# Optimization experiments

Hardware: AMD Instinct MI355X
Metric: run time of the kernel (lower is better)

The kernel has to match this reference:

```python
import jax, jax.numpy as jnp
import numpy as np

# constants matching init_kwargs
WINDOW_SHAPE = (16, 16, 8)   # (win_x, win_y, win_z)
GROUP_SIZE = 128
SHIFT = False


def setup_inputs() -> dict:
    rng = np.random.default_rng(0)
    batch_size = 16
    # ragged per-batch voxel counts, deliberately not multiples of GROUP_SIZE
    counts = 90000 + (np.arange(batch_size) * 7919) % 20007
    b = np.repeat(np.arange(batch_size, dtype=np.int32), counts)
    n = int(b.shape[0])  # 1,610,007
    sparse_shape = [32, 1024, 1024]  # (z, y, x)
    z = rng.integers(0, sparse_shape[0], n, dtype=np.int32)
    y = rng.integers(0, sparse_shape[1], n, dtype=np.int32)
    x = rng.integers(0, sparse_shape[2], n, dtype=np.int32)
    coords = np.stack([b, z, y, x], axis=1).astype(np.int32)
    return {"coords": jnp.asarray(coords), "batch_size": batch_size, "sparse_shape": sparse_shape}


def _window_coors_shift_v2(coords, sparse_shape, window_shape, shift):
    sz, sy, sx = sparse_shape
    wx, wy, wz = window_shape
    if shift:
        shx, shy, shz = wx // 2, wy // 2, wz // 2
    else:
        shx, shy, shz = 0, 0, 0
    mx = int(np.ceil(sx / wx) + 1)
    my = int(np.ceil(sy / wy) + 1)
    mz = int(np.ceil(sz / wz) + 1)
    m_per_sample = mx * my * mz
    x = coords[:, 3] + shx
    y = coords[:, 2] + shy
    z = coords[:, 1] + shz
    wcx, wcy, wcz = x // wx, y // wy, z // wz
    cix, ciy, ciz = x % wx, y % wy, z % wz
    bwin_x = coords[:, 0] * m_per_sample + wcx * my * mz + wcy * mz + wcz
    bwin_y = coords[:, 0] * m_per_sample + wcy * mx * mz + wcx * mz + wcz
    coors_in_win = jnp.stack([ciz, ciy, cix], axis=-1)
    return bwin_x, bwin_y, coors_in_win


def reference(coords, batch_size, sparse_shape):
    coords = coords.astype(jnp.int32)
    n = coords.shape[0]
    g = GROUP_SIZE
    b_ids = coords[:, 0]

    # per-batch counts (coords are grouped by batch, as the torch code assumes)
    num = jax.ops.segment_sum(jnp.ones((n,), jnp.int32), b_ids, num_segments=batch_size)
    bs = jnp.concatenate([jnp.zeros((1,), jnp.int32), jnp.cumsum(num)])        # batch_start_indices
    num_p = ((num + g - 1) // g) * g                                            # padded counts
    bsp = jnp.concatenate([jnp.zeros((1,), jnp.int32), jnp.cumsum(num_p)])     # padded starts
    n_p = int(bsp[-1])  # total padded length (data-dependent; eager reference)

    # win2flat[j] = j + (bsp[b] - bs[b])  -- maps flat index to padded index
    bias_per_batch = bsp[:-1] - bs[:-1]
    win2flat = jnp.arange(n, dtype=jnp.int32) + bias_per_batch[b_ids]

    # flat2win: vectorized version of the per-batch loop
    k = jnp.arange(n_p, dtype=jnp.int32)
    b = (jnp.searchsorted(bsp, k, side='right') - 1).astype(jnp.int32)
    bias = bsp[b] - bs[b]
    num_b = num[b]
    nump_b = num_p[b]
    in_tail = (num_b != nump_b) & (k >= bsp[b] + num_b)   # padded tail of last group
    multi_group = nump_b != g
    # multi-group: copy from previous group (value k - g - bias)
    # single group: tile the real indices of this batch (value bs[b] + (k - bsp[b] - num_b) mod num_b)
    tail_val = jnp.where(multi_group,
                         k - g - bias,
                         bs[b] + jnp.mod(k - bsp[b] - num_b, jnp.maximum(num_b, 1)))
    flat2win = jnp.where(in_tail, tail_val, k - bias)

    # window/hilbert-style flattened orders
    wx, wy, wz = WINDOW_SHAPE
    bwin_x, bwin_y, ciw = _window_coors_shift_v2(coords, sparse_shape, WINDOW_SHAPE, SHIFT)
    win_vol = wx * wy * wz
    vx = bwin_x * win_vol + ciw[:, 2] * wy * wz + ciw[:, 1] * wz + ciw[:, 0]
    vy = bwin_y * win_vol + ciw[:, 1] * wx * wz + ciw[:, 2] * wz + ciw[:, 0]
    idx_x = jnp.argsort(vx).astype(jnp.int32)
    idx_y = jnp.argsort(vy).astype(jnp.int32)

    return flat2win, win2flat, idx_x, idx_y
```

## Files before the change

### kernel.cpp

```cpp
#include <hip/hip_runtime.h>
#include <stdint.h>

#define NBATCH 16
#define GRP 128
#define THREADS 256
#define TILE 2048
#define TITEMS 8
#define SCAN_CHUNK 2048
#define SCAN_ITEMS 8
#define IDXMASK 0x1FFFFFu

#define STH 512
#define SWAVES 8
#define SIT 4

#define BLOCKW 4
#define CAP 640
#define WITEMS 10
#define WSLOT 1152

typedef unsigned long long ull;

__device__ __forceinline__ int xcd_swizzle(int blk, int G) {
  const int x = blk & 7, i = blk >> 3;
  const int q = G >> 3, r = G & 7;
  return x * q + (x < r ? x : r) + i;
}

__device__ __forceinline__ unsigned int block_scan_excl(unsigned int v,
                                                        unsigned int* s) {
  const int tid = threadIdx.x;
  s[tid] = v;
  __syncthreads();
#pragma unroll
  for (int off = 1; off < THREADS; off <<= 1) {
    unsigned int x = (tid >= off) ? s[tid - off] : 0u;
    __syncthreads();
    s[tid] += x;
    __syncthreads();
  }
  return s[tid] - v;
}

__device__ __forceinline__ unsigned int wave_incl_scan(unsigned int v) {
  const int lane = threadIdx.x & 63;
#pragma unroll
  for (int off = 1; off < 64; off <<= 1) {
    const unsigned int t = __shfl_up(v, off, 64);
    if (lane >= off) v += t;
  }
  return v;
}

template <int NW>
__device__ __forceinline__ unsigned int block_scan_excl_f(unsigned int v,
                                                          unsigned int* s) {
  const int lane = threadIdx.x & 63, w = threadIdx.x >> 6;
  __syncthreads();
  const unsigned int incl = wave_incl_scan(v);
  if (lane == 63) s[w] = incl;
  __syncthreads();
  unsigned int base = 0;
#pragma unroll
  for (int i = 0; i < NW; ++i) base += (i < w) ? s[i] : 0u;
  return base + incl - v;
}

template <int R>
__device__ __forceinline__ void wave_hist_scan(unsigned int* hist) {
  constexpr int PB = R / 64;
  const int lane = threadIdx.x & 63;
  unsigned int v[PB], s = 0;
#pragma unroll
  for (int k = 0; k < PB; ++k) { v[k] = hist[lane * PB + k]; s += v[k]; }
  const unsigned int incl = wave_incl_scan(s);
  unsigned int run = incl - s;
#pragma unroll
  for (int k = 0; k < PB; ++k) { hist[lane * PB + k] = run; run += v[k]; }
}


__global__ __launch_bounds__(THREADS) void keys_both(
    const int* __restrict__ coords,
    unsigned int* __restrict__ kx, unsigned int* __restrict__ ky,
    int* __restrict__ win2flat, int* __restrict__ f2w,
    unsigned int* __restrict__ cx0, unsigned int* __restrict__ cy0,
    int* __restrict__ binfo, ull* __restrict__ desc, int desc_words,
    int n, int n_p, int NTmax) {
  __shared__ int st[NBATCH + 1], stp[NBATCH + 1];
  __shared__ int sbsp[NBATCH + 1], snum[NBATCH], snump[NBATCH];
  __shared__ unsigned int hx[256], hy[256];
  const int tid = threadIdx.x;
  const int blk = blockIdx.x;
  for (int i = blk * THREADS + tid; i < desc_words; i += gridDim.x * THREADS)
    desc[i] = 0ull;
  if (tid <= NBATCH) {
    int lo = 0, hi = n;
    while (lo < hi) {
      const int mid = (lo + hi) >> 1;
      if (coords[4 * mid] < tid) lo = mid + 1; else hi = mid;
    }
    st[tid] = lo;
  }
  hx[tid] = 0; hy[tid] = 0;
  __syncthreads();
  if (tid == 0) {
    int b = 0, tp = 0;
    for (int i = 0; i < NBATCH; ++i) {
      const int ni = st[i + 1] - st[i];
      sbsp[i] = b; snum[i] = ni;
      const int npi = (ni + GRP - 1) / GRP * GRP;
      snump[i] = npi;
      b += npi;
      stp[i] = tp; tp += (ni + TILE - 1) / TILE;
    }
    sbsp[NBATCH] = b; stp[NBATCH] = tp;
  }
  __syncthreads();
  const int NT = stp[NBATCH];
  const int t = blk;
  int b = 0;
  if (t < NT) {
#pragma unroll
    for (int j = 1; j < NBATCH; ++j) b += (t >= stp[j]) ? 1 : 0;
    const int ebase = st[b] + (t - stp[b]) * TILE;
    const int eend = min(ebase + TILE, st[b + 1]);
    const int bias = sbsp[b] - st[b];
#pragma unroll
    for (int j = 0; j < TITEMS; ++j) {
      const int i = ebase + j * THREADS + tid;
      if (i < eend) {
        const int4 c = ((const int4*)coords)[i];
        const unsigned int x = (unsigned int)c.w, y = (unsigned int)c.z,
                           z = (unsigned int)c.y;
        const unsigned int wcx = x >> 4, cix = x & 15u;
        const unsigned int wcy = y >> 4, ciy = y & 15u;
        const unsigned int wcz = z >> 3, ciz = z & 7u;
        const unsigned int keyx =
            (wcx << 19) | (wcy << 13) | (wcz << 11) | (cix << 7) | (ciy << 3) | ciz;
        const unsigned int keyy =
            (wcy << 19) | (wcx << 13) | (wcz << 11) | (ciy << 7) | (cix << 3) | ciz;
        kx[i] = keyx;
        ky[i] = keyy;
        atomicAdd(&hx[keyx >> 17], 1u);
        atomicAdd(&hy[keyy >> 17], 1u);
        win2flat[i] = i + bias;
      }
    }
  }
#pragma unroll
  for (int j = 0; j < TITEMS; ++j) {
    const int k = blk * TILE + j * THREADS + tid;
    if (k < n_p) {
      int bb = 0;
#pragma unroll
      for (int jj = 1; jj < NBATCH; ++jj) bb += (k >= sbsp[jj]) ? 1 : 0;
      const int bias = sbsp[bb] - st[bb];
      const int nb2 = snum[bb], npb = snump[bb];
      int val = k - bias;
      if (nb2 != npb && k >= sbsp[bb] + nb2) {
        if (npb != GRP) {
          val = k - GRP - bias;
        } else {
          const int m = nb2 > 1 ? nb2 : 1;
          val = st[bb] + (k - sbsp[bb] - nb2) % m;
        }
      }
      f2w[k] = val;
    }
  }
  __syncthreads();
  if (t < NT) {
    const int ntb = stp[b + 1] - stp[b];
    const int col = 256 * stp[b] + tid * ntb + (t - stp[b]);
    cx0[col] = hx[tid];
    cy0[col] = hy[tid];
  }
  if (blk == 0) {
    if (tid <= NBATCH) { binfo[tid] = st[tid]; binfo[17 + tid] = stp[tid]; }
    for (int q = NT * 256 + tid; q < NTmax * 256; q += THREADS) {
      cx0[q] = 0; cy0[q] = 0;
    }
  }
}


__global__ __launch_bounds__(THREADS) void scan_emit(
    unsigned int* __restrict__ cx, unsigned int* __restrict__ cy, int L, int NS,
    ull* __restrict__ descx, ull* __restrict__ descy,
    unsigned int* __restrict__ bsx, unsigned int* __restrict__ bsy,
    const int* __restrict__ binfo) {
  __shared__ unsigned int s[THREADS];
  __shared__ unsigned int s_base;
  __shared__ int stp[NBATCH + 1];
  const int tid = threadIdx.x;
  const int half = (blockIdx.x >= NS) ? 1 : 0;
  const int blk = blockIdx.x - half * NS;
  unsigned int* data = half ? cy : cx;
  ull* desc = half ? descy : descx;
  unsigned int* bs = half ? bsy : bsx;
  if (tid <= NBATCH) stp[tid] = binfo[17 + tid];
  const int base = blk * SCAN_CHUNK + tid * SCAN_ITEMS;
  unsigned int v[SCAN_ITEMS], sum = 0;
#pragma unroll
  for (int j = 0; j < SCAN_ITEMS; ++j) {
    const int idx = base + j;
    v[j] = (idx < L) ? data[idx] : 0u;
    sum += v[j];
  }
  const unsigned int excl = block_scan_excl(sum, s);
  const unsigned int total = s[THREADS - 1];
  if (tid == 0) {
    const ull tag = (blk == 0) ? (2ull << 32) : (1ull << 32);
    __hip_atomic_store(&desc[blk], tag | total, __ATOMIC_RELEASE,
                       __HIP_MEMORY_SCOPE_AGENT);
    if (blk == 0) s_base = 0;
  }
  if (blk > 0 && tid < 64) {
    unsigned int run = 0;
    int jb = blk - 1;
    for (;;) {
      const int j = jb - tid;
      ull d;
      if (j >= 0) {
        do {
          d = __hip_atomic_load(&desc[j], __ATOMIC_ACQUIRE,
                                __HIP_MEMORY_SCOPE_AGENT);
        } while ((d >> 32) == 0);
      } else {
        d = (2ull << 32);
      }
      const ull m2 = __ballot((d >> 32) == 2);
      const int f = m2 ? __builtin_ctzll(m2) : 64;
      unsigned int contrib = (tid <= f) ? (unsigned int)d : 0u;
#pragma unroll
      for (int o = 32; o > 0; o >>= 1) contrib += __shfl_down(contrib, o, 64);
      run += __shfl(contrib, 0, 64);
      if (m2) break;
      jb -= 64;
    }
    if (tid == 0) {
      __hip_atomic_store(&desc[blk], (2ull << 32) | (run + total),
                         __ATOMIC_RELEASE, __HIP_MEMORY_SCOPE_AGENT);
      s_base = run;
    }
  }
  __syncthreads();
  unsigned int off = s_base + excl;
  const int NTc = stp[NBATCH];
#pragma unroll
  for (int j = 0; j < SCAN_ITEMS; ++j) {
    const int idx = base + j;
    if (idx < L) {
      data[idx] = off;
      if (idx < 256 * NTc) {
        int b = 0;
        while (b < NBATCH - 1 && idx >= 256 * stp[b + 1]) ++b;
        const int ntb = stp[b + 1] - stp[b];
        const int q = idx - 256 * stp[b];
        const int d = q / ntb;
        if (q - d * ntb == 0) bs[(b << 8) | d] = off;
      }
    }
    off += v[j];
  }
}


__global__ __launch_bounds__(STH) void scatter_msb(
    const unsigned int* __restrict__ sxp, unsigned int* __restrict__ dxk,
    unsigned int* __restrict__ dxi,
    const unsigned int* __restrict__ syp, unsigned int* __restrict__ dyk,
    unsigned int* __restrict__ dyi,
    const unsigned int* __restrict__ cx, const unsigned int* __restrict__ cy,
    const int* __restrict__ binfo, int NTS) {
  __shared__ ull tile[TILE];
  __shared__ unsigned int wh[SWAVES * 256];
  __shared__ unsigned int dbase[256];
  __shared__ unsigned int sw[SWAVES];
  __shared__ int sst[NBATCH + 1], stp[NBATCH + 1];
  const int tid = threadIdx.x;
  const int lane = tid & 63;
  const int w = tid >> 6;
  const int logical = xcd_swizzle(blockIdx.x, 2 * NTS);
  const int half = (logical >= NTS) ? 1 : 0;
  const int t = logical - half * NTS;
  if (tid <= NBATCH) { sst[tid] = binfo[tid]; stp[tid] = binfo[17 + tid]; }
  for (int d = tid; d < SWAVES * 256; d += STH) wh[d] = 0u;
  __syncthreads();
  const int NT = stp[NBATCH];
  if (t >= NT) return;
  int b = 0;
#pragma unroll
  for (int j = 1; j < NBATCH; ++j) b += (t >= stp[j]) ? 1 : 0;
  const int tfirst = stp[b];
  const int ntb = stp[b + 1] - tfirst;
  const int ebase = sst[b] + (t - tfirst) * TILE;
  const int m = min(TILE, sst[b + 1] - ebase);
  const unsigned int* __restrict__ src = half ? syp : sxp;
  unsigned int* __restrict__ dk = half ? dyk : dxk;
  unsigned int* __restrict__ di = half ? dyi : dxi;
  const unsigned int* __restrict__ counts = half ? cy : cx;
  const int wbase = w * (TILE / SWAVES);

  unsigned int key[SIT];
  unsigned int meta[SIT];
#pragma unroll
  for (int j = 0; j < SIT; ++j) {
    const int l = wbase + j * 64 + lane;
    const bool valid = l < m;
    key[j] = valid ? __builtin_nontemporal_load(&src[ebase + l]) : 0u;
    const unsigned int d = key[j] >> 17;
    unsigned int r = 0;
    if (valid) r = atomicAdd(&wh[w * 256 + d], 1u);
    meta[j] = d | (r << 16);
  }
  __syncthreads();
  {
    unsigned int cwv[SWAVES], tot = 0;
    if (tid < 256) {
#pragma unroll
      for (int ww = 0; ww < SWAVES; ++ww) { cwv[ww] = wh[ww * 256 + tid]; tot += cwv[ww]; }
    }
    const unsigned int lstart = block_scan_excl_f<SWAVES>((tid < 256) ? tot : 0u, sw);
    if (tid < 256) {
      unsigned int acc = lstart;
#pragma unroll
      for (int ww = 0; ww < SWAVES; ++ww) { wh[ww * 256 + tid] = acc; acc += cwv[ww]; }
      dbase[tid] = counts[256 * tfirst + tid * ntb + (t - tfirst)] - lstart;
    }
  }
  __syncthreads();
#pragma unroll
  for (int j = 0; j < SIT; ++j) {
    const int l = wbase + j * 64 + lane;
    if (l < m) {
      const unsigned int mt = meta[j];
      tile[wh[w * 256 + (mt & 0xFFFFu)] + (mt >> 16)] =
          ((ull)key[j] << 32) | (unsigned int)(ebase + l);
    }
  }
  __syncthreads();
  for (int s2 = tid; s2 < m; s2 += STH) {
    const ull p = tile[s2];
    const unsigned int hi = (unsigned int)(p >> 32);
    const unsigned int pos = dbase[hi >> 17] + s2;
    dk[pos] = hi;
    di[pos] = (unsigned int)p;
  }
}


__global__ __launch_bounds__(THREADS) void localsort(
    const unsigned int* __restrict__ Bk, const unsigned int* __restrict__ Bi,
    const unsigned int* __restrict__ Dk, const unsigned int* __restrict__ Di,
    int* __restrict__ oix, int* __restrict__ oiy,
    const unsigned int* __restrict__ bsx, const unsigned int* __restrict__ bsy,
    int n) {
  __shared__ unsigned int lds[BLOCKW * WSLOT];
  const int tid = threadIdx.x;
  const int lane = tid & 63;
  const int w = tid >> 6;
  const int g0 = xcd_swizzle(blockIdx.x, gridDim.x) * BLOCKW + w;
  const int half = (g0 >= NBATCH * 256) ? 1 : 0;
  const int g = g0 - half * NBATCH * 256;
  const unsigned int* __restrict__ srck = half ? Dk : Bk;
  const unsigned int* __restrict__ srci = half ? Di : Bi;
  int* __restrict__ dst = half ? oiy : oix;
  const unsigned int* __restrict__ bs = half ? bsy : bsx;
  unsigned int* recB = lds + w * WSLOT;
  unsigned int* hist = recB + CAP;
  const int begin = (int)bs[g];
  const int end = (g == NBATCH * 256 - 1) ? n : (int)bs[g + 1];
  int m = end - begin;
  if (m <= 0) return;
  if (m > CAP) m = CAP;

#pragma unroll
  for (int k = 0; k < 8; ++k) hist[lane + 64 * k] = 0u;

  unsigned int keyw[WITEMS];
#pragma unroll
  for (int j = 0; j < WITEMS; ++j) {
    const int l = 64 * j + lane;
    keyw[j] = (l < m) ? (srck[begin + l] & 0x1FFFFu) : 0u;
  }

  unsigned int rnk[WITEMS];
#pragma unroll
  for (int j = 0; j < WITEMS; ++j) {
    if (64 * j >= m) break;
    const int l = 64 * j + lane;
    rnk[j] = 0;
    if (l < m) rnk[j] = atomicAdd(&hist[keyw[j] & 0x1FFu], 1u);
  }
  wave_hist_scan<512>(hist);
#pragma unroll
  for (int j = 0; j < WITEMS; ++j) {
    if (64 * j >= m) break;
    const int l = 64 * j + lane;
    if (l < m)
      recB[hist[keyw[j] & 0x1FFu] + rnk[j]] = (keyw[j] << 10) | (unsigned int)l;
  }

#pragma unroll
  for (int k = 0; k < 4; ++k) hist[lane + 64 * k] = 0u;
  unsigned int rec2[WITEMS], rnk2[WITEMS];
#pragma unroll
  for (int j = 0; j < WITEMS; ++j) {
    const int l = 64 * j + lane;
    rec2[j] = (l < m) ? recB[l] : 0u;
  }
#pragma unroll
  for (int j = 0; j < WITEMS; ++j) {
    if (64 * j >= m) break;
    const int l = 64 * j + lane;
    rnk2[j] = 0;
    if (l < m) rnk2[j] = atomicAdd(&hist[rec2[j] >> 19], 1u);
  }
  wave_hist_scan<256>(hist);
#pragma unroll
  for (int j = 0; j < WITEMS; ++j) {
    if (64 * j >= m) break;
    const int l = 64 * j + lane;
    if (l < m) recB[hist[rec2[j] >> 19] + rnk2[j]] = rec2[j];
  }

#pragma unroll
  for (int j = 0; j < WITEMS; ++j) {
    if (64 * j >= m) break;
    const int l = 64 * j + lane;
    if (l < m) {
      const unsigned int p = recB[l] & 0x3FFu;
      dst[begin + l] = (int)srci[begin + (int)p];
    }
  }
}


static inline int ceil_div(int a, int b) { return (a + b - 1) / b; }

extern "C" void kernel_launch(void* const* d_in, const int* in_sizes, int n_in,
                              void* d_out, int out_size, void* d_ws, size_t ws_size,
                              hipStream_t stream) {
  const int* coords = (const int*)d_in[0];
  const int n = in_sizes[0] / 4;
  const int n_p = out_size - 3 * n;

  int* out = (int*)d_out;
  int* flat2win = out;
  int* win2flat = out + n_p;
  int* idx_x = out + (size_t)n_p + n;
  int* idx_y = out + (size_t)n_p + 2 * (size_t)n;

  const int NBH = ceil_div(n, TILE);
  const int NTmax = NBH + NBATCH;
  const int gridK = (NTmax > ceil_div(n_p, TILE)) ? NTmax : ceil_div(n_p, TILE);
  const int L8 = 256 * NTmax;
  const int NS8 = ceil_div(L8, SCAN_CHUNK);
  const int desc_words = 2 * NS8;
  const int LSBLK = (2 * NBATCH * 256) / BLOCKW;

  char* ws = (char*)d_ws;
  size_t off = 0;
  auto take = [&](size_t bytes) -> void* {
    void* p = (void*)(ws + off);
    off += (bytes + 255) & ~(size_t)255;
    return p;
  };
  unsigned int* A  = (unsigned int*)take((size_t)n * 4);
  unsigned int* C  = (unsigned int*)take((size_t)n * 4);
  unsigned int* Bk = (unsigned int*)take((size_t)n * 4);
  unsigned int* Bi = (unsigned int*)take((size_t)n * 4);
  unsigned int* Dk = (unsigned int*)take((size_t)n * 4);
  unsigned int* Di = (unsigned int*)take((size_t)n * 4);
  unsigned int* cx0 = (unsigned int*)take((size_t)L8 * 4);
  unsigned int* cy0 = (unsigned int*)take((size_t)L8 * 4);
  ull* desc = (ull*)take((size_t)desc_words * 8);
  unsigned int* bsx = (unsigned int*)take(4096 * 4);
  unsigned int* bsy = (unsigned int*)take(4096 * 4);
  int* binfo = (int*)take(64 * 4);
  (void)ws_size; (void)n_in;

  keys_both<<<gridK, THREADS, 0, stream>>>(coords, A, C, win2flat, flat2win,
                                           cx0, cy0, binfo, desc, desc_words,
                                           n, n_p, NTmax);
  scan_emit<<<2 * NS8, THREADS, 0, stream>>>(cx0, cy0, L8, NS8, desc, desc + NS8,
                                             bsx, bsy, binfo);
  scatter_msb<<<2 * NTmax, STH, 0, stream>>>(A, Bk, Bi, C, Dk, Di, cx0, cy0,
                                             binfo, NTmax);
  localsort<<<LSBLK, THREADS, 0, stream>>>(Bk, Bi, Dk, Di, idx_x, idx_y,
                                           bsx, bsy, n);
}
```

Baseline: 147.3 us.

## Store key/index pairs as interleaved 64-bit records and scatter directly in localsort

The MSB scatter pass now writes each key and its source index together as one 64-bit word instead of two separate 32-bit arrays, so each element costs one wider store. The local sort reads the key from the upper half of these records. Its final pass writes each output index straight to its sorted position rather than first writing the rank back to LDS and re-reading it. This removes one LDS round trip and one pass, but the global output stores become scattered within each bucket, and the key loads now read twice as many bytes.

```diff
diff --git a/kernel.cpp b/kernel.cpp
--- a/kernel.cpp
+++ b/kernel.cpp
@@ -268,10 +268,8 @@
 
 
 __global__ __launch_bounds__(STH) void scatter_msb(
-    const unsigned int* __restrict__ sxp, unsigned int* __restrict__ dxk,
-    unsigned int* __restrict__ dxi,
-    const unsigned int* __restrict__ syp, unsigned int* __restrict__ dyk,
-    unsigned int* __restrict__ dyi,
+    const unsigned int* __restrict__ sxp, ull* __restrict__ dx,
+    const unsigned int* __restrict__ syp, ull* __restrict__ dy,
     const unsigned int* __restrict__ cx, const unsigned int* __restrict__ cy,
     const int* __restrict__ binfo, int NTS) {
   __shared__ ull tile[TILE];
@@ -298,8 +296,7 @@
   const int ebase = sst[b] + (t - tfirst) * TILE;
   const int m = min(TILE, sst[b + 1] - ebase);
   const unsigned int* __restrict__ src = half ? syp : sxp;
-  unsigned int* __restrict__ dk = half ? dyk : dxk;
-  unsigned int* __restrict__ di = half ? dyi : dxi;
+  ull* __restrict__ dst = half ? dy : dx;
   const unsigned int* __restrict__ counts = half ? cy : cx;
   const int wbase = w * (TILE / SWAVES);
 
@@ -344,16 +341,13 @@
   for (int s2 = tid; s2 < m; s2 += STH) {
     const ull p = tile[s2];
     const unsigned int hi = (unsigned int)(p >> 32);
-    const unsigned int pos = dbase[hi >> 17] + s2;
-    dk[pos] = hi;
-    di[pos] = (unsigned int)p;
+    dst[dbase[hi >> 17] + s2] = p;
   }
 }
 
 
 __global__ __launch_bounds__(THREADS) void localsort(
-    const unsigned int* __restrict__ Bk, const unsigned int* __restrict__ Bi,
-    const unsigned int* __restrict__ Dk, const unsigned int* __restrict__ Di,
+    const ull* __restrict__ Bx, const ull* __restrict__ Dx,
     int* __restrict__ oix, int* __restrict__ oiy,
     const unsigned int* __restrict__ bsx, const unsigned int* __restrict__ bsy,
     int n) {
@@ -364,8 +358,7 @@
   const int g0 = xcd_swizzle(blockIdx.x, gridDim.x) * BLOCKW + w;
   const int half = (g0 >= NBATCH * 256) ? 1 : 0;
   const int g = g0 - half * NBATCH * 256;
-  const unsigned int* __restrict__ srck = half ? Dk : Bk;
-  const unsigned int* __restrict__ srci = half ? Di : Bi;
+  const ull* __restrict__ srcA = half ? Dx : Bx;
   int* __restrict__ dst = half ? oiy : oix;
   const unsigned int* __restrict__ bs = half ? bsy : bsx;
   unsigned int* recB = lds + w * WSLOT;
@@ -383,7 +376,7 @@
 #pragma unroll
   for (int j = 0; j < WITEMS; ++j) {
     const int l = 64 * j + lane;
-    keyw[j] = (l < m) ? (srck[begin + l] & 0x1FFFFu) : 0u;
+    keyw[j] = (l < m) ? ((unsigned int)(srcA[begin + l] >> 32) & 0x1FFFFu) : 0u;
   }
 
   unsigned int rnk[WITEMS];
@@ -423,16 +416,10 @@
   for (int j = 0; j < WITEMS; ++j) {
     if (64 * j >= m) break;
     const int l = 64 * j + lane;
-    if (l < m) recB[hist[rec2[j] >> 19] + rnk2[j]] = rec2[j];
-  }
-
-#pragma unroll
-  for (int j = 0; j < WITEMS; ++j) {
-    if (64 * j >= m) break;
-    const int l = 64 * j + lane;
     if (l < m) {
-      const unsigned int p = recB[l] & 0x3FFu;
-      dst[begin + l] = (int)srci[begin + (int)p];
+      const unsigned int pos = hist[rec2[j] >> 19] + rnk2[j];
+      const unsigned int p = rec2[j] & 0x3FFu;
+      dst[begin + (int)pos] = (int)(unsigned int)srcA[begin + (int)p];
     }
   }
 }
@@ -468,12 +455,10 @@
     off += (bytes + 255) & ~(size_t)255;
     return p;
   };
-  unsigned int* A  = (unsigned int*)take((size_t)n * 4);
-  unsigned int* C  = (unsigned int*)take((size_t)n * 4);
-  unsigned int* Bk = (unsigned int*)take((size_t)n * 4);
-  unsigned int* Bi = (unsigned int*)take((size_t)n * 4);
-  unsigned int* Dk = (unsigned int*)take((size_t)n * 4);
-  unsigned int* Di = (unsigned int*)take((size_t)n * 4);
+  unsigned int* A = (unsigned int*)take((size_t)n * 4);
+  unsigned int* C = (unsigned int*)take((size_t)n * 4);
+  ull* B = (ull*)take((size_t)n * 8);
+  ull* D = (ull*)take((size_t)n * 8);
   unsigned int* cx0 = (unsigned int*)take((size_t)L8 * 4);
   unsigned int* cy0 = (unsigned int*)take((size_t)L8 * 4);
   ull* desc = (ull*)take((size_t)desc_words * 8);
@@ -487,8 +472,7 @@
                                            n, n_p, NTmax);
   scan_emit<<<2 * NS8, THREADS, 0, stream>>>(cx0, cy0, L8, NS8, desc, desc + NS8,
                                              bsx, bsy, binfo);
-  scatter_msb<<<2 * NTmax, STH, 0, stream>>>(A, Bk, Bi, C, Dk, Di, cx0, cy0,
-                                             binfo, NTmax);
-  localsort<<<LSBLK, THREADS, 0, stream>>>(Bk, Bi, Dk, Di, idx_x, idx_y,
-                                           bsx, bsy, n);
-}
+  scatter_msb<<<2 * NTmax, STH, 0, stream>>>(A, B, C, D, cx0, cy0, binfo,
+                                             NTmax);
+  localsort<<<LSBLK, THREADS, 0, stream>>>(B, D, idx_x, idx_y, bsx, bsy, n);
+}
```

Result: slower. 150.5 us (+2.1%).
